# Kernel tuning notes

Measured on AMD Instinct MI355X. Metric: run time of the kernel, lower is better.

## Reference

```python
import jax, jax.numpy as jnp
import numpy as np


def setup_inputs() -> dict:
    key = jax.random.key(0)
    B, S, H, O, L, NH = 16, 1024, 1024, 256, 4, 8
    ks = jax.random.split(key, 10)
    s = 0.02
    return {
        "x": jax.random.normal(ks[0], (B, S, H), dtype=jnp.float32),
        "Wf": jax.random.normal(ks[1], (L, H, H), dtype=jnp.float32) * s,
        "bf": jnp.zeros((L, H), dtype=jnp.float32),
        "Wi": jax.random.normal(ks[2], (L, H, H), dtype=jnp.float32) * s,
        "bi": jnp.zeros((L, H), dtype=jnp.float32),
        "Wh": jax.random.normal(ks[3], (L, H, H), dtype=jnp.float32) * s,
        "bh": jnp.zeros((L, H), dtype=jnp.float32),
        "in_proj_w": jax.random.normal(ks[4], (3 * H, H), dtype=jnp.float32) * s,
        "in_proj_b": jnp.zeros((3 * H,), dtype=jnp.float32),
        "out_w": jax.random.normal(ks[5], (H, H), dtype=jnp.float32) * s,
        "out_b": jnp.zeros((H,), dtype=jnp.float32),
        "fc_w": jax.random.normal(ks[6], (O, H), dtype=jnp.float32) * s,
        "fc_b": jnp.zeros((O,), dtype=jnp.float32),
    }


def _min_lstm_layer(x, Wf, bf, Wi, bi, Wh, bh):
    # x: [B, S, D] -> [B, S, H]. minLSTM: h_t = f'_t * h_{t-1} + i'_t * h~_t
    f = jax.nn.sigmoid(jnp.einsum("bsd,hd->bsh", x, Wf) + bf)
    i = jax.nn.sigmoid(jnp.einsum("bsd,hd->bsh", x, Wi) + bi)
    h_tilde = jnp.einsum("bsd,hd->bsh", x, Wh) + bh
    denom = f + i
    fp = f / denom                      # decay coefficient per step
    add = (i / denom) * h_tilde         # input contribution per step
    # sequential scan over time (linear gated recurrence)
    def step(h, inp):
        fp_t, add_t = inp               # each [B, H]
        h = fp_t * h + add_t
        return h, h
    B, S, H = fp.shape
    h0 = jnp.zeros((B, H), dtype=x.dtype)
    _, hs = jax.lax.scan(step, h0, (fp.transpose(1, 0, 2), add.transpose(1, 0, 2)))
    return hs.transpose(1, 0, 2)        # [B, S, H]


def _mhsa(x, in_proj_w, in_proj_b, out_w, out_b, num_heads=8):
    B, S, H = x.shape
    dh = H // num_heads
    qkv = jnp.einsum("bsh,oh->bso", x, in_proj_w) + in_proj_b  # [B,S,3H]
    q, k, v = jnp.split(qkv, 3, axis=-1)
    def heads(t):
        return t.reshape(B, S, num_heads, dh).transpose(0, 2, 1, 3)  # [B,nh,S,dh]
    q, k, v = heads(q), heads(k), heads(v)
    scores = jnp.einsum("bnqd,bnkd->bnqk", q, k) / jnp.sqrt(jnp.float32(dh)).astype(x.dtype)
    attn = jax.nn.softmax(scores, axis=-1)
    o = jnp.einsum("bnqk,bnkd->bnqd", attn, v)
    o = o.transpose(0, 2, 1, 3).reshape(B, S, H)
    return jnp.einsum("bsh,oh->bso", o, out_w) + out_b


def reference(x, Wf, bf, Wi, bi, Wh, bh, in_proj_w, in_proj_b, out_w, out_b, fc_w, fc_b):
    out = x
    L = Wf.shape[0]
    for l in range(L):
        out = _min_lstm_layer(out, Wf[l], bf[l], Wi[l], bi[l], Wh[l], bh[l])
    attn_out = _mhsa(out, in_proj_w, in_proj_b, out_w, out_b, num_heads=8)
    out = attn_out + out                 # dropout is identity at eval
    last = out[:, -1, :]                 # [B, H]
    return jnp.einsum("bh,oh->bo", last, fc_w) + fc_b
```

## Files before the change

### kernel.cpp

```cpp
#include <hip/hip_runtime.h>
#include <hip/hip_bf16.h>
#include <math.h>

#define Bq   16
#define Sq   1024
#define Hq   1024
#define Oq   256
#define Lq   4
#define NHq  8
#define DHq  128
#define Mq   (Bq*Sq)
#define HHq  (Hq*Hq)
#define NCc  32
#define CTc  32

typedef __bf16 bf16x8 __attribute__((ext_vector_type(8)));
typedef float  f32x4  __attribute__((ext_vector_type(4)));

__device__ __forceinline__ float bf2f(unsigned int u) {
    union { unsigned int i; float f; } x; x.i = u << 16; return x.f;
}
__device__ __forceinline__ unsigned short f2bf(float f) {
    union { float f; unsigned int i; } x; x.f = f;
    unsigned int r = x.i + 0x7fffu + ((x.i >> 16) & 1u);
    return (unsigned short)(r >> 16);
}
__device__ __forceinline__ float sigm(float x) { return 1.f / (1.f + __expf(-x)); }

__device__ __forceinline__ void gl2lds16(const unsigned short* g, unsigned short* l) {
    __builtin_amdgcn_global_load_lds((const __attribute__((address_space(1))) void*)g,
                                     (__attribute__((address_space(3))) void*)l, 16, 0, 0);
}

__global__ void cvt_kernel(const float* __restrict__ src, unsigned short* __restrict__ dst, int n) {
    int i = blockIdx.x * 256 + threadIdx.x;
    if (i < n) dst[i] = f2bf(src[i]);
}

__global__ void cvtW_kernel(const float* __restrict__ Wf, const float* __restrict__ Wi,
                            const float* __restrict__ Wh, unsigned short* __restrict__ Wcat) {
    int i = blockIdx.x * 256 + threadIdx.x;
    int l = (i >> 20) / 3;
    int r = i - l * 3 * HHq;
    int g = r >> 20; int j = r & (HHq - 1);
    const float* s = (g == 0) ? Wf : (g == 1) ? Wi : Wh;
    Wcat[i] = f2bf(s[(size_t)l * HHq + j]);
}

__global__ void bias3_kernel(const float* __restrict__ bf_, const float* __restrict__ bi_,
                             const float* __restrict__ bh_, float* __restrict__ out) {
    int i = blockIdx.x * 256 + threadIdx.x;
    int l = i / (3*Hq); int r = i % (3*Hq); int g = r >> 10; int j = r & (Hq-1);
    const float* s = (g == 0) ? bf_ : (g == 1) ? bi_ : bh_;
    out[i] = s[l*Hq + j];
}

__global__ __launch_bounds__(256, 2)
void gemm_gate_kernel(const unsigned short* __restrict__ A, const unsigned short* __restrict__ Wl,
                      const float* __restrict__ bias3, unsigned short* __restrict__ FPo,
                      unsigned short* __restrict__ ADDo)
{
    const int K = Hq;
    __shared__ unsigned short lds[4 * 10240];
    const int tid  = threadIdx.x;

    const int lid = blockIdx.x;
    const int xcd = lid & 7;
    const int s   = lid >> 3;
    const int bm  = xcd * 16 + (s >> 4);
    const int cb  = s & 15;

    const int wid  = tid >> 6, lane = tid & 63;
    const int wm   = (wid >> 1) * 64;
    const int wn   = (wid & 1) * 32;
    const int l15  = lane & 15, quad = lane >> 4;

    const unsigned short* Ag = A + (size_t)(bm*128) * K;

    const int lr   = lane >> 2;
    const int gc   = (lane & 3) ^ ((lane >> 3) & 3);
    int offA[2], ldsA[2];
    #pragma unroll
    for (int q = 0; q < 2; ++q) {
        int ra = wid*32 + q*16 + lr;
        offA[q] = ra * K + gc*8;
        ldsA[q] = (wid*32 + q*16) * 32;
    }
    int offW[3], ldsW[3];
    #pragma unroll
    for (int q = 0; q < 3; ++q) {
        int rw = wid*48 + q*16 + lr;
        int g  = rw >> 6;
        int nr = rw & 63;
        offW[q] = g * HHq + (cb*64 + nr) * K + gc*8;
        ldsW[q] = 4096 + (wid*48 + q*16) * 32;
    }

    const int crd = quad ^ ((l15 >> 1) & 3);

    f32x4 acc[3][4][2] = {};

    auto STAGE = [&](int kt, int slot) {
        const int kof = kt << 5;
        unsigned short* Sb = &lds[slot * 10240];
        #pragma unroll
        for (int q = 0; q < 2; ++q) gl2lds16(Ag + offA[q] + kof, Sb + ldsA[q]);
        #pragma unroll
        for (int q = 0; q < 3; ++q) gl2lds16(Wl + offW[q] + kof, Sb + ldsW[q]);
    };

    auto COMPUTE = [&](int slot) {
        const unsigned short* Sa = &lds[slot * 10240];
        const unsigned short* Sw = Sa + 4096;
        bf16x8 af[4];
        #pragma unroll
        for (int t = 0; t < 4; ++t)
            af[t] = *(const bf16x8*)&Sa[(wm + t*16 + l15)*32 + crd*8];
        bf16x8 wf[3][2];
        #pragma unroll
        for (int g = 0; g < 3; ++g)
            #pragma unroll
            for (int t = 0; t < 2; ++t)
                wf[g][t] = *(const bf16x8*)&Sw[(g*64 + wn + t*16 + l15)*32 + crd*8];
        __builtin_amdgcn_s_setprio(1);
        #pragma unroll
        for (int g = 0; g < 3; ++g)
            #pragma unroll
            for (int tm = 0; tm < 4; ++tm)
                #pragma unroll
                for (int tn = 0; tn < 2; ++tn)
                    acc[g][tm][tn] = __builtin_amdgcn_mfma_f32_16x16x32_bf16(af[tm], wf[g][tn], acc[g][tm][tn], 0, 0, 0);
        __builtin_amdgcn_s_setprio(0);
    };

    const int niter = K >> 5;

    STAGE(0, 0);
    STAGE(1, 1);

    for (int t = 0; t < niter - 2; ++t) {
        STAGE(t + 2, (t + 2) & 3);
        asm volatile("s_waitcnt vmcnt(10) lgkmcnt(0)" ::: "memory");
        __builtin_amdgcn_s_barrier();
        asm volatile("" ::: "memory");
        COMPUTE(t & 3);
    }
    asm volatile("s_waitcnt vmcnt(5) lgkmcnt(0)" ::: "memory");
    __builtin_amdgcn_s_barrier();
    asm volatile("" ::: "memory");
    COMPUTE((niter - 2) & 3);
    asm volatile("s_waitcnt vmcnt(0) lgkmcnt(0)" ::: "memory");
    __builtin_amdgcn_s_barrier();
    asm volatile("" ::: "memory");
    COMPUTE((niter - 1) & 3);

    #pragma unroll
    for (int tm = 0; tm < 4; ++tm) {
        int row0 = bm*128 + wm + tm*16 + quad*4;
        #pragma unroll
        for (int tn = 0; tn < 2; ++tn) {
            int col = cb*64 + wn + tn*16 + l15;
            float bf_ = bias3[col], bi_ = bias3[Hq + col], bh_ = bias3[2*Hq + col];
            #pragma unroll
            for (int r = 0; r < 4; ++r) {
                float f  = sigm(acc[0][tm][tn][r] + bf_);
                float i  = sigm(acc[1][tm][tn][r] + bi_);
                float ht = acc[2][tm][tn][r] + bh_;
                float rd = 1.f / (f + i);
                size_t off = (size_t)(row0 + r) * Hq + col;
                FPo[off]  = f2bf(f * rd);
                ADDo[off] = f2bf(i * rd * ht);
            }
        }
    }
}

__global__ __launch_bounds__(256, 2)
void gemm_bt_kernel(const unsigned short* __restrict__ A, const unsigned short* __restrict__ W,
                    const float* __restrict__ bias, unsigned short* __restrict__ C,
                    int N, int K, int nbn)
{
    __shared__ unsigned short lds[4 * 8192];
    const int tid  = threadIdx.x;

    const int lid = blockIdx.x;
    const int xcd = lid & 7;
    const int s   = lid >> 3;
    const int bm  = xcd * 16 + s / nbn;
    const int bn  = s % nbn;

    const int wid  = tid >> 6, lane = tid & 63;
    const int wm   = (wid >> 1) * 64, wn = (wid & 1) * 64;
    const int l15  = lane & 15, quad = lane >> 4;

    const unsigned short* Ag = A + (size_t)(bm*128) * K;
    const unsigned short* Wg = W + (size_t)(bn*128) * K;

    const int r0   = wid*32 + (lane >> 2);
    const int cst  = (lane & 3) ^ ((r0 >> 1) & 3);
    const int g0   = r0 * K + cst*8;
    const int g1   = (r0 + 16) * K + cst*8;
    const int lofs0 = wid*1024;
    const int lofs1 = wid*1024 + 512;

    const int crd = quad ^ ((l15 >> 1) & 3);

    f32x4 acc[4][4] = {};

    auto STAGE = [&](int kt, int slot) {
        const int kof = kt << 5;
        unsigned short* Sb = &lds[slot * 8192];
        gl2lds16(Ag + g0 + kof, Sb + lofs0);
        gl2lds16(Ag + g1 + kof, Sb + lofs1);
        gl2lds16(Wg + g0 + kof, Sb + 4096 + lofs0);
        gl2lds16(Wg + g1 + kof, Sb + 4096 + lofs1);
    };

    auto COMPUTE = [&](int slot) {
        const unsigned short* Sa = &lds[slot * 8192];
        const unsigned short* Sw = Sa + 4096;
        bf16x8 af[4], wf[4];
        #pragma unroll
        for (int t = 0; t < 4; ++t) {
            af[t] = *(const bf16x8*)&Sa[(wm + t*16 + l15)*32 + crd*8];
            wf[t] = *(const bf16x8*)&Sw[(wn + t*16 + l15)*32 + crd*8];
        }
        __builtin_amdgcn_s_setprio(1);
        #pragma unroll
        for (int tm = 0; tm < 4; ++tm)
            #pragma unroll
            for (int tn = 0; tn < 4; ++tn)
                acc[tm][tn] = __builtin_amdgcn_mfma_f32_16x16x32_bf16(af[tm], wf[tn], acc[tm][tn], 0, 0, 0);
        __builtin_amdgcn_s_setprio(0);
    };

    const int niter = K >> 5;

    STAGE(0, 0);
    STAGE(1, 1);

    for (int it = 0; it < niter - 2; ++it) {
        STAGE(it + 2, (it + 2) & 3);
        asm volatile("s_waitcnt vmcnt(8) lgkmcnt(0)" ::: "memory");
        __builtin_amdgcn_s_barrier();
        asm volatile("" ::: "memory");
        COMPUTE(it & 3);
    }
    asm volatile("s_waitcnt vmcnt(4) lgkmcnt(0)" ::: "memory");
    __builtin_amdgcn_s_barrier();
    asm volatile("" ::: "memory");
    COMPUTE((niter - 2) & 3);
    asm volatile("s_waitcnt vmcnt(0) lgkmcnt(0)" ::: "memory");
    __builtin_amdgcn_s_barrier();
    asm volatile("" ::: "memory");
    COMPUTE((niter - 1) & 3);

    #pragma unroll
    for (int tm = 0; tm < 4; ++tm) {
        int row0 = bm*128 + wm + tm*16 + quad*4;
        #pragma unroll
        for (int tn = 0; tn < 4; ++tn) {
            int col = bn*128 + wn + tn*16 + l15;
            float bv = bias[col];
            #pragma unroll
            for (int r = 0; r < 4; ++r)
                C[(size_t)(row0 + r) * N + col] = f2bf(acc[tm][tn][r] + bv);
        }
    }
}

__global__ __launch_bounds__(256)
void scan_sum_kernel(const unsigned short* __restrict__ FP, const unsigned short* __restrict__ AD,
                     float* __restrict__ Ps, float* __restrict__ Asum) {
    int bid = blockIdx.x;
    int tid = threadIdx.x;
    int b = bid >> 6; int r = bid & 63; int chunk = r >> 1; int jb = r & 1;
    int j = jb*512 + tid*2;
    size_t base = ((size_t)(b*Sq + chunk*CTc)) * Hq + j;
    float P0 = 1.f, P1 = 1.f, A0 = 0.f, A1 = 0.f;
    for (int s = 0; s < CTc; ++s) {
        size_t ro = base + (size_t)s * Hq;
        unsigned int uf = *(const unsigned int*)(FP + ro);
        unsigned int ua = *(const unsigned int*)(AD + ro);
        float fp0 = bf2f(uf & 0xffffu), fp1 = bf2f(uf >> 16);
        float ad0 = bf2f(ua & 0xffffu), ad1 = bf2f(ua >> 16);
        P0 *= fp0; A0 = fp0 * A0 + ad0;
        P1 *= fp1; A1 = fp1 * A1 + ad1;
    }
    int oi = (b*NCc + chunk)*Hq + j;
    Ps[oi] = P0; Ps[oi+1] = P1;
    Asum[oi] = A0; Asum[oi+1] = A1;
}

__global__ void scan_base_kernel(const float* __restrict__ Ps, const float* __restrict__ Asum,
                                 float* __restrict__ Hb) {
    int t = blockIdx.x * 256 + threadIdx.x;
    int b = t >> 10, j = t & 1023;
    float h = 0.f;
    for (int c = 0; c < NCc; ++c) {
        int idx = (b*NCc + c)*Hq + j;
        Hb[idx] = h;
        h = Ps[idx] * h + Asum[idx];
    }
}

__global__ __launch_bounds__(256)
void scan_out_kernel(const unsigned short* __restrict__ FP, const unsigned short* __restrict__ AD,
                     const float* __restrict__ Hb, unsigned short* __restrict__ Ho) {
    int bid = blockIdx.x;
    int tid = threadIdx.x;
    int b = bid >> 6; int r = bid & 63; int chunk = r >> 1; int jb = r & 1;
    int j = jb*512 + tid*2;
    size_t base = ((size_t)(b*Sq + chunk*CTc)) * Hq + j;
    int oi = (b*NCc + chunk)*Hq + j;
    float h0 = Hb[oi], h1 = Hb[oi+1];
    for (int s = 0; s < CTc; ++s) {
        size_t ro = base + (size_t)s * Hq;
        unsigned int uf = *(const unsigned int*)(FP + ro);
        unsigned int ua = *(const unsigned int*)(AD + ro);
        h0 = bf2f(uf & 0xffffu) * h0 + bf2f(ua & 0xffffu);
        h1 = bf2f(uf >> 16)     * h1 + bf2f(ua >> 16);
        unsigned int packed = (unsigned int)f2bf(h0) | ((unsigned int)f2bf(h1) << 16);
        *(unsigned int*)(Ho + ro) = packed;
    }
}

__global__ void xlast_kernel(const unsigned short* __restrict__ act, float* __restrict__ xl) {
    int i = blockIdx.x * 256 + threadIdx.x;
    int b = i >> 10, j = i & 1023;
    xl[i] = bf2f((unsigned int)act[((size_t)(b*Sq + Sq-1)) * Hq + j]);
}

__global__ __launch_bounds__(256)
void gemv_kernel(const float* __restrict__ W, const float* __restrict__ xv,
                 const float* __restrict__ bias, const float* __restrict__ resid,
                 float* __restrict__ out, int N) {
    int b = blockIdx.x;
    int w = threadIdx.x >> 6, lane = threadIdx.x & 63;
    int n = blockIdx.y*4 + w;
    __shared__ float xs[Hq];
    *(float4*)&xs[threadIdx.x*4] = *(const float4*)&xv[(size_t)b*Hq + threadIdx.x*4];
    __syncthreads();
    const float4* wr = (const float4*)(W + (size_t)n * Hq);
    float a = 0.f;
    #pragma unroll
    for (int c = 0; c < 4; ++c) {
        float4 wv = wr[c*64 + lane];
        float4 x4 = *(const float4*)&xs[c*256 + lane*4];
        a += wv.x*x4.x + wv.y*x4.y + wv.z*x4.z + wv.w*x4.w;
    }
    #pragma unroll
    for (int st = 32; st > 0; st >>= 1) a += __shfl_xor(a, st, 64);
    if (lane == 0) out[(size_t)b*N + n] = a + bias[n] + (resid ? resid[(size_t)b*Hq + n] : 0.f);
}

__global__ __launch_bounds__(1024)
void attn_kernel(const unsigned short* __restrict__ KV,
                 const float* __restrict__ q, float* __restrict__ o) {
    int b = blockIdx.x >> 3, nh = blockIdx.x & 7;
    int tid = threadIdx.x;
    __shared__ float qs[DHq];
    __shared__ float p[Sq];
    __shared__ float redw[16];
    __shared__ float red2[16*DHq];
    if (tid < DHq) qs[tid] = q[b*Hq + nh*DHq + tid] * 0.08838834764831845f;
    __syncthreads();

    const int g = tid >> 4, l = tid & 15;
    const unsigned short* Kb = KV + (size_t)b*Sq*2048 + nh*DHq;
    float lmax = -1e30f;
    #pragma unroll 4
    for (int it = 0; it < 16; ++it) {
        int s = it*64 + g;
        union { uint4 v; unsigned short u[8]; } kk;
        kk.v = *(const uint4*)(Kb + (size_t)s*2048 + l*8);
        float a = 0.f;
        #pragma unroll
        for (int j = 0; j < 8; ++j) a += bf2f((unsigned int)kk.u[j]) * qs[l*8 + j];
        a += __shfl_xor(a, 1, 16);
        a += __shfl_xor(a, 2, 16);
        a += __shfl_xor(a, 4, 16);
        a += __shfl_xor(a, 8, 16);
        if (l == 0) p[s] = a;
        lmax = fmaxf(lmax, a);
    }
    #pragma unroll
    for (int st = 32; st > 0; st >>= 1) lmax = fmaxf(lmax, __shfl_xor(lmax, st, 64));
    if ((tid & 63) == 0) redw[tid >> 6] = lmax;
    __syncthreads();
    float mx = redw[0];
    #pragma unroll
    for (int i = 1; i < 16; ++i) mx = fmaxf(mx, redw[i]);

    float e = __expf(p[tid] - mx);
    float ls = e;
    #pragma unroll
    for (int st = 32; st > 0; st >>= 1) ls += __shfl_xor(ls, st, 64);
    __syncthreads();
    p[tid] = e;
    if ((tid & 63) == 0) redw[tid >> 6] = ls;
    __syncthreads();
    float ssum = 0.f;
    #pragma unroll
    for (int i = 0; i < 16; ++i) ssum += redw[i];
    float inv = 1.f / ssum;

    int d2 = (tid & 63) * 2, sb = tid >> 6;
    const unsigned short* Vb = KV + (size_t)b*Sq*2048 + 1024 + nh*DHq + d2;
    float a0 = 0.f, a1 = 0.f;
    for (int s = sb*64; s < sb*64 + 64; ++s) {
        unsigned int vv = *(const unsigned int*)(Vb + (size_t)s*2048);
        float pw = p[s];
        a0 += pw * bf2f(vv & 0xffffu);
        a1 += pw * bf2f(vv >> 16);
    }
    red2[sb*DHq + d2] = a0;
    red2[sb*DHq + d2 + 1] = a1;
    __syncthreads();
    if (tid < DHq) {
        float a = 0.f;
        #pragma unroll
        for (int i = 0; i < 16; ++i) a += red2[i*DHq + tid];
        o[b*Hq + nh*DHq + tid] = a * inv;
    }
}

extern "C" void kernel_launch(void* const* d_in, const int* in_sizes, int n_in,
                              void* d_out, int out_size, void* d_ws, size_t ws_size,
                              hipStream_t stream) {
    const float* x        = (const float*)d_in[0];
    const float* Wf       = (const float*)d_in[1];
    const float* bfv      = (const float*)d_in[2];
    const float* Wi       = (const float*)d_in[3];
    const float* biv      = (const float*)d_in[4];
    const float* Wh       = (const float*)d_in[5];
    const float* bhv      = (const float*)d_in[6];
    const float* in_proj_w= (const float*)d_in[7];
    const float* in_proj_b= (const float*)d_in[8];
    const float* out_w    = (const float*)d_in[9];
    const float* out_b    = (const float*)d_in[10];
    const float* fc_w     = (const float*)d_in[11];
    const float* fc_b     = (const float*)d_in[12];
    float* outp = (float*)d_out;

    char* p = (char*)d_ws;
    auto alloc = [&](size_t bytes) -> void* {
        void* r = (void*)p; p += (bytes + 255) & ~(size_t)255; return r;
    };
    unsigned short* Wcat = (unsigned short*)alloc((size_t)Lq*3*HHq*2);
    unsigned short* Wkv  = (unsigned short*)alloc((size_t)2048*Hq*2);
    float*          Bias3= (float*)alloc((size_t)Lq*3*Hq*4);
    unsigned short* actA = (unsigned short*)alloc((size_t)Mq*Hq*2);
    unsigned short* actB = (unsigned short*)alloc((size_t)Mq*Hq*2);
    unsigned short* FPg  = (unsigned short*)alloc((size_t)Mq*Hq*2);
    unsigned short* ADDg = (unsigned short*)alloc((size_t)Mq*Hq*2);
    float* Ps   = (float*)alloc((size_t)Bq*NCc*Hq*4);
    float* Asum = (float*)alloc((size_t)Bq*NCc*Hq*4);
    float* Hb   = (float*)alloc((size_t)Bq*NCc*Hq*4);
    unsigned short* KV = FPg;
    float* xl   = (float*)alloc((size_t)Bq*Hq*4);
    float* qbuf = (float*)alloc((size_t)Bq*Hq*4);
    float* obuf = (float*)alloc((size_t)Bq*Hq*4);
    float* rbuf = (float*)alloc((size_t)Bq*Hq*4);

    cvt_kernel<<<Mq*Hq/256, 256, 0, stream>>>(x, actA, Mq*Hq);
    cvtW_kernel<<<Lq*3*HHq/256, 256, 0, stream>>>(Wf, Wi, Wh, Wcat);
    cvt_kernel<<<2048*Hq/256, 256, 0, stream>>>(in_proj_w + (size_t)Hq*Hq, Wkv, 2048*Hq);
    bias3_kernel<<<(Lq*3*Hq)/256, 256, 0, stream>>>(bfv, biv, bhv, Bias3);

    unsigned short* cur = actA;
    unsigned short* nxt = actB;
    for (int l = 0; l < Lq; ++l) {
        gemm_gate_kernel<<<(Mq/128)*16, 256, 0, stream>>>(
            cur, Wcat + (size_t)l*3*HHq, Bias3 + l*3*Hq, FPg, ADDg);
        scan_sum_kernel<<<Bq*NCc*2, 256, 0, stream>>>(FPg, ADDg, Ps, Asum);
        scan_base_kernel<<<Bq*Hq/256, 256, 0, stream>>>(Ps, Asum, Hb);
        scan_out_kernel<<<Bq*NCc*2, 256, 0, stream>>>(FPg, ADDg, Hb, nxt);
        unsigned short* t = cur; cur = nxt; nxt = t;
    }

    gemm_bt_kernel<<<(Mq/128)*(2048/128), 256, 0, stream>>>(
        cur, Wkv, in_proj_b + Hq, KV, 2048, Hq, 2048/128);
    xlast_kernel<<<Bq*Hq/256, 256, 0, stream>>>(cur, xl);
    gemv_kernel<<<dim3(Bq, Hq/4), 256, 0, stream>>>(in_proj_w, xl, in_proj_b, nullptr, qbuf, Hq);
    attn_kernel<<<Bq*NHq, 1024, 0, stream>>>(KV, qbuf, obuf);
    gemv_kernel<<<dim3(Bq, Hq/4), 256, 0, stream>>>(out_w, obuf, out_b, xl, rbuf, Hq);
    gemv_kernel<<<dim3(Bq, Oq/4), 256, 0, stream>>>(fc_w, rbuf, fc_b, nullptr, outp, Oq);
}
```

Baseline: 891.4 us.

## Enlarge GEMM block tiles and switch to double-buffered LDS pipeline

Both GEMM kernels now give each block a wider N tile: the gate GEMM covers 128 columns per gate and the KV GEMM covers 256 columns. Each wave computes all 128 rows over a narrower column slice, so accumulators double. The LDS pipeline drops from four stages with two-ahead prefetch to two stages with one-ahead prefetch, plus a second barrier per iteration. The goal is more reuse of each A and W tile and less global traffic per FLOP, at the cost of higher register pressure, fewer blocks and less latency hiding.

```diff
diff --git a/kernel.cpp b/kernel.cpp
--- a/kernel.cpp
+++ b/kernel.cpp
@@ -61,18 +61,17 @@
                       unsigned short* __restrict__ ADDo)
 {
     const int K = Hq;
-    __shared__ unsigned short lds[4 * 10240];
+    __shared__ unsigned short lds[2 * 16384];
     const int tid  = threadIdx.x;
 
     const int lid = blockIdx.x;
     const int xcd = lid & 7;
     const int s   = lid >> 3;
-    const int bm  = xcd * 16 + (s >> 4);
-    const int cb  = s & 15;
+    const int bm  = xcd * 16 + (s >> 3);
+    const int cb  = s & 7;
 
     const int wid  = tid >> 6, lane = tid & 63;
-    const int wm   = (wid >> 1) * 64;
-    const int wn   = (wid & 1) * 32;
+    const int wn   = wid * 32;
     const int l15  = lane & 15, quad = lane >> 4;
 
     const unsigned short* Ag = A + (size_t)(bm*128) * K;
@@ -86,80 +85,76 @@
         offA[q] = ra * K + gc*8;
         ldsA[q] = (wid*32 + q*16) * 32;
     }
-    int offW[3], ldsW[3];
-    #pragma unroll
-    for (int q = 0; q < 3; ++q) {
-        int rw = wid*48 + q*16 + lr;
-        int g  = rw >> 6;
-        int nr = rw & 63;
-        offW[q] = g * HHq + (cb*64 + nr) * K + gc*8;
-        ldsW[q] = 4096 + (wid*48 + q*16) * 32;
+    int offW[6], ldsW[6];
+    #pragma unroll
+    for (int q = 0; q < 6; ++q) {
+        int rw = wid*96 + q*16 + lr;
+        int g  = rw >> 7;
+        int nr = rw & 127;
+        offW[q] = g * HHq + (cb*128 + nr) * K + gc*8;
+        ldsW[q] = 4096 + (wid*96 + q*16) * 32;
     }
 
     const int crd = quad ^ ((l15 >> 1) & 3);
 
-    f32x4 acc[3][4][2] = {};
+    f32x4 acc[3][8][2] = {};
 
     auto STAGE = [&](int kt, int slot) {
         const int kof = kt << 5;
-        unsigned short* Sb = &lds[slot * 10240];
+        unsigned short* Sb = &lds[slot * 16384];
         #pragma unroll
         for (int q = 0; q < 2; ++q) gl2lds16(Ag + offA[q] + kof, Sb + ldsA[q]);
         #pragma unroll
-        for (int q = 0; q < 3; ++q) gl2lds16(Wl + offW[q] + kof, Sb + ldsW[q]);
+        for (int q = 0; q < 6; ++q) gl2lds16(Wl + offW[q] + kof, Sb + ldsW[q]);
     };
 
     auto COMPUTE = [&](int slot) {
-        const unsigned short* Sa = &lds[slot * 10240];
+        const unsigned short* Sa = &lds[slot * 16384];
         const unsigned short* Sw = Sa + 4096;
-        bf16x8 af[4];
-        #pragma unroll
-        for (int t = 0; t < 4; ++t)
-            af[t] = *(const bf16x8*)&Sa[(wm + t*16 + l15)*32 + crd*8];
-        bf16x8 wf[3][2];
-        #pragma unroll
-        for (int g = 0; g < 3; ++g)
+        bf16x8 af[8];
+        #pragma unroll
+        for (int t = 0; t < 8; ++t)
+            af[t] = *(const bf16x8*)&Sa[(t*16 + l15)*32 + crd*8];
+        __builtin_amdgcn_s_setprio(1);
+        #pragma unroll
+        for (int g = 0; g < 3; ++g) {
+            bf16x8 wf[2];
             #pragma unroll
             for (int t = 0; t < 2; ++t)
-                wf[g][t] = *(const bf16x8*)&Sw[(g*64 + wn + t*16 + l15)*32 + crd*8];
-        __builtin_amdgcn_s_setprio(1);
-        #pragma unroll
-        for (int g = 0; g < 3; ++g)
+                wf[t] = *(const bf16x8*)&Sw[(g*128 + wn + t*16 + l15)*32 + crd*8];
             #pragma unroll
-            for (int tm = 0; tm < 4; ++tm)
+            for (int tm = 0; tm < 8; ++tm)
                 #pragma unroll
                 for (int tn = 0; tn < 2; ++tn)
-                    acc[g][tm][tn] = __builtin_amdgcn_mfma_f32_16x16x32_bf16(af[tm], wf[g][tn], acc[g][tm][tn], 0, 0, 0);
+                    acc[g][tm][tn] = __builtin_amdgcn_mfma_f32_16x16x32_bf16(af[tm], wf[tn], acc[g][tm][tn], 0, 0, 0);
+        }
         __builtin_amdgcn_s_setprio(0);
     };
 
     const int niter = K >> 5;
 
     STAGE(0, 0);
-    STAGE(1, 1);
-
-    for (int t = 0; t < niter - 2; ++t) {
-        STAGE(t + 2, (t + 2) & 3);
-        asm volatile("s_waitcnt vmcnt(10) lgkmcnt(0)" ::: "memory");
+    for (int t = 0; t < niter - 1; ++t) {
+        STAGE(t + 1, (t + 1) & 1);
+        asm volatile("s_waitcnt vmcnt(8) lgkmcnt(0)" ::: "memory");
         __builtin_amdgcn_s_barrier();
         asm volatile("" ::: "memory");
-        COMPUTE(t & 3);
-    }
-    asm volatile("s_waitcnt vmcnt(5) lgkmcnt(0)" ::: "memory");
-    __builtin_amdgcn_s_barrier();
-    asm volatile("" ::: "memory");
-    COMPUTE((niter - 2) & 3);
+        COMPUTE(t & 1);
+        asm volatile("" ::: "memory");
+        __builtin_amdgcn_s_barrier();
+        asm volatile("" ::: "memory");
+    }
     asm volatile("s_waitcnt vmcnt(0) lgkmcnt(0)" ::: "memory");
     __builtin_amdgcn_s_barrier();
     asm volatile("" ::: "memory");
-    COMPUTE((niter - 1) & 3);
-
-    #pragma unroll
-    for (int tm = 0; tm < 4; ++tm) {
-        int row0 = bm*128 + wm + tm*16 + quad*4;
+    COMPUTE((niter - 1) & 1);
+
+    #pragma unroll
+    for (int tm = 0; tm < 8; ++tm) {
+        int row0 = bm*128 + tm*16 + quad*4;
         #pragma unroll
         for (int tn = 0; tn < 2; ++tn) {
-            int col = cb*64 + wn + tn*16 + l15;
+            int col = cb*128 + wn + tn*16 + l15;
             float bf_ = bias3[col], bi_ = bias3[Hq + col], bh_ = bias3[2*Hq + col];
             #pragma unroll
             for (int r = 0; r < 4; ++r) {
@@ -180,7 +175,7 @@
                     const float* __restrict__ bias, unsigned short* __restrict__ C,
                     int N, int K, int nbn)
 {
-    __shared__ unsigned short lds[4 * 8192];
+    __shared__ unsigned short lds[2 * 12288];
     const int tid  = threadIdx.x;
 
     const int lid = blockIdx.x;
@@ -190,44 +185,54 @@
     const int bn  = s % nbn;
 
     const int wid  = tid >> 6, lane = tid & 63;
-    const int wm   = (wid >> 1) * 64, wn = (wid & 1) * 64;
+    const int wn   = wid * 64;
     const int l15  = lane & 15, quad = lane >> 4;
 
     const unsigned short* Ag = A + (size_t)(bm*128) * K;
-    const unsigned short* Wg = W + (size_t)(bn*128) * K;
-
-    const int r0   = wid*32 + (lane >> 2);
-    const int cst  = (lane & 3) ^ ((r0 >> 1) & 3);
-    const int g0   = r0 * K + cst*8;
-    const int g1   = (r0 + 16) * K + cst*8;
-    const int lofs0 = wid*1024;
-    const int lofs1 = wid*1024 + 512;
+
+    const int lr   = lane >> 2;
+    const int gc   = (lane & 3) ^ ((lane >> 3) & 3);
+    int offA[2], ldsA[2];
+    #pragma unroll
+    for (int q = 0; q < 2; ++q) {
+        int ra = wid*32 + q*16 + lr;
+        offA[q] = ra * K + gc*8;
+        ldsA[q] = (wid*32 + q*16) * 32;
+    }
+    int offW[4], ldsW[4];
+    #pragma unroll
+    for (int q = 0; q < 4; ++q) {
+        int rw = wid*64 + q*16 + lr;
+        offW[q] = (bn*256 + rw) * K + gc*8;
+        ldsW[q] = 4096 + (wid*64 + q*16) * 32;
+    }
 
     const int crd = quad ^ ((l15 >> 1) & 3);
 
-    f32x4 acc[4][4] = {};
+    f32x4 acc[8][4] = {};
 
     auto STAGE = [&](int kt, int slot) {
         const int kof = kt << 5;
-        unsigned short* Sb = &lds[slot * 8192];
-        gl2lds16(Ag + g0 + kof, Sb + lofs0);
-        gl2lds16(Ag + g1 + kof, Sb + lofs1);
-        gl2lds16(Wg + g0 + kof, Sb + 4096 + lofs0);
-        gl2lds16(Wg + g1 + kof, Sb + 4096 + lofs1);
+        unsigned short* Sb = &lds[slot * 12288];
+        #pragma unroll
+        for (int q = 0; q < 2; ++q) gl2lds16(Ag + offA[q] + kof, Sb + ldsA[q]);
+        #pragma unroll
+        for (int q = 0; q < 4; ++q) gl2lds16(W + offW[q] + kof, Sb + ldsW[q]);
     };
 
     auto COMPUTE = [&](int slot) {
-        const unsigned short* Sa = &lds[slot * 8192];
+        const unsigned short* Sa = &lds[slot * 12288];
         const unsigned short* Sw = Sa + 4096;
-        bf16x8 af[4], wf[4];
-        #pragma unroll
-        for (int t = 0; t < 4; ++t) {
-            af[t] = *(const bf16x8*)&Sa[(wm + t*16 + l15)*32 + crd*8];
+        bf16x8 af[8], wf[4];
+        #pragma unroll
+        for (int t = 0; t < 8; ++t)
+            af[t] = *(const bf16x8*)&Sa[(t*16 + l15)*32 + crd*8];
+        #pragma unroll
+        for (int t = 0; t < 4; ++t)
             wf[t] = *(const bf16x8*)&Sw[(wn + t*16 + l15)*32 + crd*8];
-        }
         __builtin_amdgcn_s_setprio(1);
         #pragma unroll
-        for (int tm = 0; tm < 4; ++tm)
+        for (int tm = 0; tm < 8; ++tm)
             #pragma unroll
             for (int tn = 0; tn < 4; ++tn)
                 acc[tm][tn] = __builtin_amdgcn_mfma_f32_16x16x32_bf16(af[tm], wf[tn], acc[tm][tn], 0, 0, 0);
@@ -237,30 +242,27 @@
     const int niter = K >> 5;
 
     STAGE(0, 0);
-    STAGE(1, 1);
-
-    for (int it = 0; it < niter - 2; ++it) {
-        STAGE(it + 2, (it + 2) & 3);
-        asm volatile("s_waitcnt vmcnt(8) lgkmcnt(0)" ::: "memory");
+    for (int it = 0; it < niter - 1; ++it) {
+        STAGE(it + 1, (it + 1) & 1);
+        asm volatile("s_waitcnt vmcnt(6) lgkmcnt(0)" ::: "memory");
         __builtin_amdgcn_s_barrier();
         asm volatile("" ::: "memory");
-        COMPUTE(it & 3);
-    }
-    asm volatile("s_waitcnt vmcnt(4) lgkmcnt(0)" ::: "memory");
-    __builtin_amdgcn_s_barrier();
-    asm volatile("" ::: "memory");
-    COMPUTE((niter - 2) & 3);
+        COMPUTE(it & 1);
+        asm volatile("" ::: "memory");
+        __builtin_amdgcn_s_barrier();
+        asm volatile("" ::: "memory");
+    }
     asm volatile("s_waitcnt vmcnt(0) lgkmcnt(0)" ::: "memory");
     __builtin_amdgcn_s_barrier();
     asm volatile("" ::: "memory");
-    COMPUTE((niter - 1) & 3);
-
-    #pragma unroll
-    for (int tm = 0; tm < 4; ++tm) {
-        int row0 = bm*128 + wm + tm*16 + quad*4;
+    COMPUTE((niter - 1) & 1);
+
+    #pragma unroll
+    for (int tm = 0; tm < 8; ++tm) {
+        int row0 = bm*128 + tm*16 + quad*4;
         #pragma unroll
         for (int tn = 0; tn < 4; ++tn) {
-            int col = bn*128 + wn + tn*16 + l15;
+            int col = bn*256 + wn + tn*16 + l15;
             float bv = bias[col];
             #pragma unroll
             for (int r = 0; r < 4; ++r)
@@ -471,7 +473,7 @@
     unsigned short* cur = actA;
     unsigned short* nxt = actB;
     for (int l = 0; l < Lq; ++l) {
-        gemm_gate_kernel<<<(Mq/128)*16, 256, 0, stream>>>(
+        gemm_gate_kernel<<<(Mq/128)*(Hq/128), 256, 0, stream>>>(
             cur, Wcat + (size_t)l*3*HHq, Bias3 + l*3*Hq, FPg, ADDg);
         scan_sum_kernel<<<Bq*NCc*2, 256, 0, stream>>>(FPg, ADDg, Ps, Asum);
         scan_base_kernel<<<Bq*Hq/256, 256, 0, stream>>>(Ps, Asum, Hb);
@@ -479,8 +481,8 @@
         unsigned short* t = cur; cur = nxt; nxt = t;
     }
 
-    gemm_bt_kernel<<<(Mq/128)*(2048/128), 256, 0, stream>>>(
-        cur, Wkv, in_proj_b + Hq, KV, 2048, Hq, 2048/128);
+    gemm_bt_kernel<<<(Mq/128)*(2048/256), 256, 0, stream>>>(
+        cur, Wkv, in_proj_b + Hq, KV, 2048, Hq, 2048/256);
     xlast_kernel<<<Bq*Hq/256, 256, 0, stream>>>(cur, xl);
     gemv_kernel<<<dim3(Bq, Hq/4), 256, 0, stream>>>(in_proj_w, xl, in_proj_b, nullptr, qbuf, Hq);
     attn_kernel<<<Bq*NHq, 1024, 0, stream>>>(KV, qbuf, obuf);
```

New measurement: 973.3 us. 1.09x slower.
